# Performance work log

Measured on AMD Instinct MI355X. Metric: run time of the kernel, lower is better.

The kernel has to match this reference:

```python
import jax, jax.numpy as jnp
import numpy as np


def setup_inputs() -> dict:
    key = jax.random.key(0)
    k1, k2 = jax.random.split(key)
    N, C = 16384, 4096
    x = jax.random.normal(k1, (N, C), dtype=jnp.float32)
    y = jax.random.randint(k2, (N, C), 0, 2, dtype=jnp.int64)
    return {"x": x, "y": y}


def reference(x, y):
    # Original loss: for each row i,
    #   loss_i = 1/(ni*(C-ni)) * sum_{j: y=1, k: y=0} exp(-(x_k - x_j))
    # which factorizes exactly into separable masked row sums:
    #   loss_i = (sum_{y=1} exp(x)) * (sum_{y=0} exp(-x)) / (ni*(C-ni))
    C = x.shape[1]
    m = (y == 1)
    pos = jnp.sum(jnp.where(m, jnp.exp(x), 0.0), axis=1)   # sum exp(x) over y==1
    neg = jnp.sum(jnp.where(m, 0.0, jnp.exp(-x)), axis=1)  # sum exp(-x) over y==0
    ni = jnp.sum(m, axis=1).astype(x.dtype)
    loss = jnp.mean(pos * neg / (ni * (C - ni)))
    return loss
```

## Files before the change

### kernel.cpp

```cpp
#include <hip/hip_runtime.h>


#define C_DIM 4096
#define BLOCK 256
#define NBLK  2048
#define WAVES_PER_BLOCK (BLOCK / 64)

__global__ __launch_bounds__(BLOCK) void pdl_rows(const float* __restrict__ x,
                                                  const int* __restrict__ y,
                                                  float* __restrict__ partial,
                                                  int rows_per_wave) {
    const int lane = threadIdx.x & 63;
    const int wave = threadIdx.x >> 6;
    const int gwave = blockIdx.x * WAVES_PER_BLOCK + wave;

    float wacc = 0.0f;

    for (int r = 0; r < rows_per_wave; ++r) {
        const int row = gwave * rows_per_wave + r;
        const float4* __restrict__ x4 = (const float4*)(x + (size_t)row * C_DIM);
        const int4*  __restrict__ y4 = (const int4*)(y + (size_t)row * C_DIM);

        float pos = 0.0f, neg = 0.0f;
        int cnt = 0;

#pragma unroll
        for (int chunk = 0; chunk < 4; ++chunk) {
            float4 xv[4];
            int4  yv[4];
#pragma unroll
            for (int u = 0; u < 4; ++u) {
                const int i = lane + (chunk * 4 + u) * 64;
                xv[u] = x4[i];
                yv[u] = y4[i];
            }
#pragma unroll
            for (int u = 0; u < 4; ++u) {
                { const float e = __expf(yv[u].x ? xv[u].x : -xv[u].x);
                  pos += yv[u].x ? e : 0.0f; neg += yv[u].x ? 0.0f : e; cnt += yv[u].x; }
                { const float e = __expf(yv[u].y ? xv[u].y : -xv[u].y);
                  pos += yv[u].y ? e : 0.0f; neg += yv[u].y ? 0.0f : e; cnt += yv[u].y; }
                { const float e = __expf(yv[u].z ? xv[u].z : -xv[u].z);
                  pos += yv[u].z ? e : 0.0f; neg += yv[u].z ? 0.0f : e; cnt += yv[u].z; }
                { const float e = __expf(yv[u].w ? xv[u].w : -xv[u].w);
                  pos += yv[u].w ? e : 0.0f; neg += yv[u].w ? 0.0f : e; cnt += yv[u].w; }
            }
        }

#pragma unroll
        for (int off = 32; off >= 1; off >>= 1) {
            pos += __shfl_down(pos, off, 64);
            neg += __shfl_down(neg, off, 64);
            cnt += __shfl_down(cnt, off, 64);
        }
        if (lane == 0) {
            const float denom = (float)cnt * (float)(C_DIM - cnt);
            wacc += (pos * neg) / denom;
        }
    }

    __shared__ float sacc[WAVES_PER_BLOCK];
    if (lane == 0) sacc[wave] = wacc;
    __syncthreads();
    if (threadIdx.x == 0) {
        float b = 0.0f;
#pragma unroll
        for (int w = 0; w < WAVES_PER_BLOCK; ++w) b += sacc[w];
        partial[blockIdx.x] = b;
    }
}

__global__ __launch_bounds__(BLOCK) void pdl_reduce(const float* __restrict__ partial,
                                                    float* __restrict__ out,
                                                    float inv_n) {
    float s = 0.0f;
    for (int i = threadIdx.x; i < NBLK; i += BLOCK) s += partial[i];
#pragma unroll
    for (int off = 32; off >= 1; off >>= 1) s += __shfl_down(s, off, 64);
    __shared__ float sw[WAVES_PER_BLOCK];
    const int lane = threadIdx.x & 63;
    const int wave = threadIdx.x >> 6;
    if (lane == 0) sw[wave] = s;
    __syncthreads();
    if (threadIdx.x == 0) {
        float t = 0.0f;
#pragma unroll
        for (int w = 0; w < WAVES_PER_BLOCK; ++w) t += sw[w];
        out[0] = t * inv_n;
    }
}

extern "C" void kernel_launch(void* const* d_in, const int* in_sizes, int n_in,
                              void* d_out, int out_size, void* d_ws, size_t ws_size,
                              hipStream_t stream) {
    const float* x = (const float*)d_in[0];
    const int*   y = (const int*)d_in[1];
    float* out = (float*)d_out;
    float* partial = (float*)d_ws;

    const int n_rows = in_sizes[0] / C_DIM;
    const int rows_per_wave = n_rows / (NBLK * WAVES_PER_BLOCK);

    pdl_rows<<<NBLK, BLOCK, 0, stream>>>(x, y, partial, rows_per_wave);
    pdl_reduce<<<1, BLOCK, 0, stream>>>(partial, out, 1.0f / (float)n_rows);
}
```

Before: 497.0 us.

## Map one row per wave and double-buffer chunk loads in row kernel

The row kernel now launches one block per four rows, with each wave handling a single row instead of looping over two rows. Chunk loads are double-buffered so the next chunk's x/y loads are in flight while the current chunk is computed. The final reduce reads partials as float4 over the larger block count. This aims to raise memory-level parallelism and overlap load latency with exp work, at the cost of more blocks, more partials and higher register pressure from the two buffers.

Result: no change. 498.2 us (+0.2%).

```diff
diff --git a/kernel.cpp b/kernel.cpp
--- a/kernel.cpp
+++ b/kernel.cpp
@@ -3,81 +3,88 @@
 
 #define C_DIM 4096
 #define BLOCK 256
-#define NBLK  2048
-#define WAVES_PER_BLOCK (BLOCK / 64)
+#define WPB   (BLOCK / 64)
 
 __global__ __launch_bounds__(BLOCK) void pdl_rows(const float* __restrict__ x,
                                                   const int* __restrict__ y,
-                                                  float* __restrict__ partial,
-                                                  int rows_per_wave) {
+                                                  float* __restrict__ partial) {
     const int lane = threadIdx.x & 63;
     const int wave = threadIdx.x >> 6;
-    const int gwave = blockIdx.x * WAVES_PER_BLOCK + wave;
+    const int row  = blockIdx.x * WPB + wave;
 
-    float wacc = 0.0f;
+    const float4* __restrict__ x4 = (const float4*)(x + (size_t)row * C_DIM);
+    const int4*  __restrict__ y4 = (const int4*)(y + (size_t)row * C_DIM);
 
-    for (int r = 0; r < rows_per_wave; ++r) {
-        const int row = gwave * rows_per_wave + r;
-        const float4* __restrict__ x4 = (const float4*)(x + (size_t)row * C_DIM);
-        const int4*  __restrict__ y4 = (const int4*)(y + (size_t)row * C_DIM);
+    float pos = 0.0f, neg = 0.0f;
+    int cnt = 0;
 
-        float pos = 0.0f, neg = 0.0f;
-        int cnt = 0;
+    float4 xa[4], xb[4];
+    int4  ya[4], yb[4];
+
+    auto prefetch = [&](float4 (&xv)[4], int4 (&yv)[4], int c) {
+#pragma unroll
+        for (int u = 0; u < 4; ++u) {
+            const int i = lane + (c * 4 + u) * 64;
+            xv[u] = x4[i];
+            yv[u] = y4[i];
+        }
+    };
+    auto compute = [&](const float4 (&xv)[4], const int4 (&yv)[4]) {
+#pragma unroll
+        for (int u = 0; u < 4; ++u) {
+            { const float e = __expf(yv[u].x ? xv[u].x : -xv[u].x);
+              pos += yv[u].x ? e : 0.0f; neg += yv[u].x ? 0.0f : e; cnt += yv[u].x; }
+            { const float e = __expf(yv[u].y ? xv[u].y : -xv[u].y);
+              pos += yv[u].y ? e : 0.0f; neg += yv[u].y ? 0.0f : e; cnt += yv[u].y; }
+            { const float e = __expf(yv[u].z ? xv[u].z : -xv[u].z);
+              pos += yv[u].z ? e : 0.0f; neg += yv[u].z ? 0.0f : e; cnt += yv[u].z; }
+            { const float e = __expf(yv[u].w ? xv[u].w : -xv[u].w);
+              pos += yv[u].w ? e : 0.0f; neg += yv[u].w ? 0.0f : e; cnt += yv[u].w; }
+        }
+    };
+
+    prefetch(xa, ya, 0);
+    prefetch(xb, yb, 1);
+    compute(xa, ya);
+    prefetch(xa, ya, 2);
+    compute(xb, yb);
+    prefetch(xb, yb, 3);
+    compute(xa, ya);
+    compute(xb, yb);
 
 #pragma unroll
-        for (int chunk = 0; chunk < 4; ++chunk) {
-            float4 xv[4];
-            int4  yv[4];
-#pragma unroll
-            for (int u = 0; u < 4; ++u) {
-                const int i = lane + (chunk * 4 + u) * 64;
-                xv[u] = x4[i];
-                yv[u] = y4[i];
-            }
-#pragma unroll
-            for (int u = 0; u < 4; ++u) {
-                { const float e = __expf(yv[u].x ? xv[u].x : -xv[u].x);
-                  pos += yv[u].x ? e : 0.0f; neg += yv[u].x ? 0.0f : e; cnt += yv[u].x; }
-                { const float e = __expf(yv[u].y ? xv[u].y : -xv[u].y);
-                  pos += yv[u].y ? e : 0.0f; neg += yv[u].y ? 0.0f : e; cnt += yv[u].y; }
-                { const float e = __expf(yv[u].z ? xv[u].z : -xv[u].z);
-                  pos += yv[u].z ? e : 0.0f; neg += yv[u].z ? 0.0f : e; cnt += yv[u].z; }
-                { const float e = __expf(yv[u].w ? xv[u].w : -xv[u].w);
-                  pos += yv[u].w ? e : 0.0f; neg += yv[u].w ? 0.0f : e; cnt += yv[u].w; }
-            }
-        }
-
-#pragma unroll
-        for (int off = 32; off >= 1; off >>= 1) {
-            pos += __shfl_down(pos, off, 64);
-            neg += __shfl_down(neg, off, 64);
-            cnt += __shfl_down(cnt, off, 64);
-        }
-        if (lane == 0) {
-            const float denom = (float)cnt * (float)(C_DIM - cnt);
-            wacc += (pos * neg) / denom;
-        }
+    for (int off = 32; off >= 1; off >>= 1) {
+        pos += __shfl_down(pos, off, 64);
+        neg += __shfl_down(neg, off, 64);
+        cnt += __shfl_down(cnt, off, 64);
     }
 
-    __shared__ float sacc[WAVES_PER_BLOCK];
-    if (lane == 0) sacc[wave] = wacc;
+    __shared__ float sacc[WPB];
+    if (lane == 0) {
+        const float denom = (float)cnt * (float)(C_DIM - cnt);
+        sacc[wave] = (pos * neg) / denom;
+    }
     __syncthreads();
     if (threadIdx.x == 0) {
         float b = 0.0f;
 #pragma unroll
-        for (int w = 0; w < WAVES_PER_BLOCK; ++w) b += sacc[w];
+        for (int w = 0; w < WPB; ++w) b += sacc[w];
         partial[blockIdx.x] = b;
     }
 }
 
 __global__ __launch_bounds__(BLOCK) void pdl_reduce(const float* __restrict__ partial,
                                                     float* __restrict__ out,
-                                                    float inv_n) {
+                                                    int n_partial, float inv_n) {
+    const float4* p4 = (const float4*)partial;
     float s = 0.0f;
-    for (int i = threadIdx.x; i < NBLK; i += BLOCK) s += partial[i];
+    for (int i = threadIdx.x; i < n_partial / 4; i += BLOCK) {
+        const float4 v = p4[i];
+        s += (v.x + v.y) + (v.z + v.w);
+    }
 #pragma unroll
     for (int off = 32; off >= 1; off >>= 1) s += __shfl_down(s, off, 64);
-    __shared__ float sw[WAVES_PER_BLOCK];
+    __shared__ float sw[WPB];
     const int lane = threadIdx.x & 63;
     const int wave = threadIdx.x >> 6;
     if (lane == 0) sw[wave] = s;
@@ -85,7 +92,7 @@
     if (threadIdx.x == 0) {
         float t = 0.0f;
 #pragma unroll
-        for (int w = 0; w < WAVES_PER_BLOCK; ++w) t += sw[w];
+        for (int w = 0; w < WPB; ++w) t += sw[w];
         out[0] = t * inv_n;
     }
 }
@@ -98,9 +105,9 @@
     float* out = (float*)d_out;
     float* partial = (float*)d_ws;
 
-    const int n_rows = in_sizes[0] / C_DIM;
-    const int rows_per_wave = n_rows / (NBLK * WAVES_PER_BLOCK);
+    const int n_rows  = in_sizes[0] / C_DIM;
+    const int n_blocks = n_rows / WPB;
 
-    pdl_rows<<<NBLK, BLOCK, 0, stream>>>(x, y, partial, rows_per_wave);
-    pdl_reduce<<<1, BLOCK, 0, stream>>>(partial, out, 1.0f / (float)n_rows);
+    pdl_rows<<<n_blocks, BLOCK, 0, stream>>>(x, y, partial);
+    pdl_reduce<<<1, BLOCK, 0, stream>>>(partial, out, n_blocks, 1.0f / (float)n_rows);
 }
```
